# Kernel tuning notes

Hardware: AMD Instinct MI355X
Metric: run time of the kernel (lower is better)

The kernel has to match this reference:

```python
import jax, jax.numpy as jnp
import numpy as np
import math

B, T, D, H = 2, 2048, 1024, 16
HD = D // H
EPS = 1e-5


def layer_norm(x, gamma, beta):
    mu = jnp.mean(x, axis=-1, keepdims=True)
    var = jnp.mean(jnp.square(x - mu), axis=-1, keepdims=True)
    return (x - mu) * jax.lax.rsqrt(var + EPS) * gamma + beta


def setup_inputs() -> dict:
    key = jax.random.key(0)
    ks = jax.random.split(key, 12)
    s = 0.02
    return {
        "x": jax.random.normal(ks[0], (B, T, D), dtype=jnp.float32),
        # weights stored [in, out] (apply as x @ W)
        "w_qkv": jax.random.normal(ks[1], (D, 3 * D), dtype=jnp.float32) * s,
        "w_out": jax.random.normal(ks[2], (D, D), dtype=jnp.float32) * s,
        "w_ff1": jax.random.normal(ks[3], (D, 4 * D), dtype=jnp.float32) * s,
        "b_ff1": jnp.zeros((4 * D,), dtype=jnp.float32),
        "w_ff2": jax.random.normal(ks[4], (4 * D, D), dtype=jnp.float32) * s,
        "b_ff2": jnp.zeros((D,), dtype=jnp.float32),
        "g1": jnp.ones((D,), dtype=jnp.float32),
        "be1": jnp.zeros((D,), dtype=jnp.float32),
        "g2": jnp.ones((D,), dtype=jnp.float32),
        "be2": jnp.zeros((D,), dtype=jnp.float32),
    }


def reference(x, w_qkv, w_out, w_ff1, b_ff1, w_ff2, b_ff2, g1, be1, g2, be2):
    residual = x
    xn = layer_norm(x, g1, be1)
    qkv = (xn @ w_qkv).reshape(B, T, 3, H, HD)
    q, k, v = jnp.moveaxis(qkv, 2, 0)          # each [B, T, H, HD]
    scale = 1.0 / math.sqrt(HD)
    attn = jnp.einsum("bqhd,bkhd->bhqk", q, k) * scale  # [B,H,T,T]
    attn = jax.nn.softmax(attn, axis=-1)
    out = jnp.einsum("bhqk,bkhd->bqhd", attn, v).reshape(B, T, D)
    out = out @ w_out
    x = residual + out
    residual = x
    xn = layer_norm(x, g2, be2)
    h = jax.nn.gelu(xn @ w_ff1 + b_ff1, approximate=False)  # torch nn.GELU = exact erf
    x = residual + (h @ w_ff2 + b_ff2)
    return x
```

## Files before the change

### kernel.cpp

```cpp
#include <hip/hip_runtime.h>
#include <math.h>

#define Bc 2
#define Tc 2048
#define Dc 1024
#define Hc 16
#define HDc 64
#define Mc (Bc * Tc)

typedef __attribute__((ext_vector_type(4))) float f32x4;
typedef __attribute__((ext_vector_type(8))) short bf16x8;

__device__ __forceinline__ unsigned short f2bf(float f) {
  unsigned int u = __float_as_uint(f);
  u += 0x7fff + ((u >> 16) & 1);
  return (unsigned short)(u >> 16);
}

__device__ __forceinline__ void gload16(const void* g, void* l) {
  __builtin_amdgcn_global_load_lds((const __attribute__((address_space(1))) unsigned int*)g,
                                   (__attribute__((address_space(3))) unsigned int*)l, 16, 0, 0);
}

__global__ __launch_bounds__(256) void wconv_kernel(const float* __restrict__ W,
                                                    unsigned short* __restrict__ Wt,
                                                    int K, int N) {
  __shared__ float tile[64][65];
  const int t = threadIdx.x;
  const int kt = blockIdx.y * 64, nt = blockIdx.x * 64;
#pragma unroll
  for (int p = 0; p < 4; p++) {
    int kr = p * 16 + (t >> 4);
    int nc = (t & 15) * 4;
    float4 v = *(const float4*)&W[(size_t)(kt + kr) * N + nt + nc];
    tile[kr][nc] = v.x; tile[kr][nc + 1] = v.y; tile[kr][nc + 2] = v.z; tile[kr][nc + 3] = v.w;
  }
  __syncthreads();
  const int nr = t >> 2, kc = (t & 3) * 16;
  unsigned int u[8];
#pragma unroll
  for (int i = 0; i < 8; i++)
    u[i] = (unsigned int)f2bf(tile[kc + 2 * i][nr]) | ((unsigned int)f2bf(tile[kc + 2 * i + 1][nr]) << 16);
  uint4 w0; w0.x = u[0]; w0.y = u[1]; w0.z = u[2]; w0.w = u[3];
  uint4 w1; w1.x = u[4]; w1.y = u[5]; w1.z = u[6]; w1.w = u[7];
  *(uint4*)&Wt[(size_t)(nt + nr) * K + kt + kc] = w0;
  *(uint4*)&Wt[(size_t)(nt + nr) * K + kt + kc + 8] = w1;
}

__global__ __launch_bounds__(256) void ln_kernel(const float* __restrict__ x,
                                                 const float* __restrict__ g,
                                                 const float* __restrict__ be,
                                                 unsigned short* __restrict__ out) {
  const int row = blockIdx.x;
  const int t = threadIdx.x;
  const float4* xp = (const float4*)(x + (size_t)row * Dc);
  float4 v = xp[t];
  float s = v.x + v.y + v.z + v.w;
  float s2 = v.x * v.x + v.y * v.y + v.z * v.z + v.w * v.w;
#pragma unroll
  for (int off = 32; off; off >>= 1) {
    s += __shfl_down(s, off);
    s2 += __shfl_down(s2, off);
  }
  __shared__ float rs[4], rs2[4];
  if ((t & 63) == 0) { rs[t >> 6] = s; rs2[t >> 6] = s2; }
  __syncthreads();
  float S = rs[0] + rs[1] + rs[2] + rs[3];
  float S2 = rs2[0] + rs2[1] + rs2[2] + rs2[3];
  float mean = S * (1.0f / Dc);
  float var = S2 * (1.0f / Dc) - mean * mean;
  float rstd = rsqrtf(var + 1e-5f);
  float4 gv = ((const float4*)g)[t];
  float4 bv = ((const float4*)be)[t];
  float o0 = (v.x - mean) * rstd * gv.x + bv.x;
  float o1 = (v.y - mean) * rstd * gv.y + bv.y;
  float o2 = (v.z - mean) * rstd * gv.z + bv.z;
  float o3 = (v.w - mean) * rstd * gv.w + bv.w;
  uint2 pk;
  pk.x = (unsigned int)f2bf(o0) | ((unsigned int)f2bf(o1) << 16);
  pk.y = (unsigned int)f2bf(o2) | ((unsigned int)f2bf(o3) << 16);
  *(uint2*)(out + (size_t)row * Dc + t * 4) = pk;
}

#define GBM 128
#define GBN 128
#define GBK 32

__global__ __launch_bounds__(256) void gemm_bf16(const unsigned short* __restrict__ A,
                                                 const unsigned short* __restrict__ Wt,
                                                 const float* __restrict__ bias,
                                                 const float* __restrict__ resid,
                                                 float* __restrict__ C,
                                                 unsigned short* __restrict__ aux,
                                                 int M, int N, int K, int flags) {
  __shared__ alignas(16) unsigned short As[GBM][GBK];
  __shared__ alignas(16) unsigned short Bs[GBN][GBK];
  const int t = threadIdx.x;
  const int lane = t & 63, wave = t >> 6;
  const int wr = wave >> 1, wc = wave & 1;
  const int c = lane & 15, g = lane >> 4;
  const int row0 = blockIdx.y * GBM, col0 = blockIdx.x * GBN;

  f32x4 acc[4][4];
#pragma unroll
  for (int m = 0; m < 4; m++)
#pragma unroll
    for (int n = 0; n < 4; n++) acc[m][n] = (f32x4){0.f, 0.f, 0.f, 0.f};

  char* AsB = (char*)&As[0][0];
  char* BsB = (char*)&Bs[0][0];
  const int l0 = t, l1 = t + 256;
  const int lds0 = wave * 1024, lds1 = wave * 1024 + 4096;

  for (int k0 = 0; k0 < K; k0 += GBK) {
    gload16(A + (size_t)(row0 + (l0 >> 2)) * K + k0 + (l0 & 3) * 8, AsB + lds0);
    gload16(A + (size_t)(row0 + (l1 >> 2)) * K + k0 + (l1 & 3) * 8, AsB + lds1);
    gload16(Wt + (size_t)(col0 + (l0 >> 2)) * K + k0 + (l0 & 3) * 8, BsB + lds0);
    gload16(Wt + (size_t)(col0 + (l1 >> 2)) * K + k0 + (l1 & 3) * 8, BsB + lds1);
    __syncthreads();
    bf16x8 af[4], bfv[4];
#pragma unroll
    for (int m = 0; m < 4; m++) af[m] = *(const bf16x8*)(AsB + (wr * 64 + m * 16 + c) * 64 + g * 16);
#pragma unroll
    for (int n = 0; n < 4; n++) bfv[n] = *(const bf16x8*)(BsB + (wc * 64 + n * 16 + c) * 64 + g * 16);
#pragma unroll
    for (int m = 0; m < 4; m++)
#pragma unroll
      for (int n = 0; n < 4; n++)
        acc[m][n] = __builtin_amdgcn_mfma_f32_16x16x32_bf16(af[m], bfv[n], acc[m][n], 0, 0, 0);
    __syncthreads();
  }

#pragma unroll
  for (int m = 0; m < 4; m++) {
    const int row = row0 + wr * 64 + m * 16 + g * 4;
#pragma unroll
    for (int n = 0; n < 4; n++) {
      const int col = col0 + wc * 64 + n * 16 + c;
      const float bi = (flags & 1) ? bias[col] : 0.0f;
#pragma unroll
      for (int r = 0; r < 4; r++) {
        float v = acc[m][n][r] + bi;
        if (flags & 2) v = 0.5f * v * (1.0f + erff(v * 0.70710678118654752f));
        if (flags & 4) v += resid[(size_t)(row + r) * N + col];
        if (flags & 16) {
          int rr = row + r;
          int b = rr >> 11, tt = rr & 2047;
          int s = col >> 10, wcol = col & 1023;
          int h = wcol >> 6, f = wcol & 63;
          size_t base = ((size_t)(b * Hc + h)) * 131072;
          unsigned short bv = f2bf(v);
          if (s == 0) {
            aux[base + (size_t)tt * HDc + f] = bv;
          } else if (s == 1) {
            aux[4194304 + base + (size_t)(tt >> 4) * 1024 + (f >> 3) * 128 + (tt & 15) * 8 + (f & 7)] = bv;
          } else {
            int kk = tt & 63;
            aux[8388608 + base + (size_t)(tt >> 6) * 4096 + (f >> 4) * 1024 +
                ((kk >> 5) & 1) * 512 + ((kk >> 3) & 3) * 128 + (f & 15) * 8 + (kk & 7)] = bv;
          }
        } else if (flags & 8) {
          aux[(size_t)(row + r) * N + col] = f2bf(v);
        } else {
          C[(size_t)(row + r) * N + col] = v;
        }
      }
    }
  }
}

__global__ __launch_bounds__(256, 4) void fattn(const unsigned short* __restrict__ Qb,
                                                const unsigned short* __restrict__ KF,
                                                const unsigned short* __restrict__ VF,
                                                unsigned short* __restrict__ Ob) {
  __shared__ alignas(16) unsigned short P[4][16][64];
  const int t = threadIdx.x, wave = t >> 6, lane = t & 63;
  const int c = lane & 15, g = lane >> 4;
  const int bid = blockIdx.x;
  const int bh = ((bid & 7) << 2) | ((bid >> 3) & 3);
  const int qt = bid >> 5;
  const int q0 = qt * 64 + wave * 16;

  const unsigned short* Qp = Qb + ((size_t)bh * Tc + q0) * HDc;
  const unsigned short* Kp = KF + (size_t)bh * 131072;
  const unsigned short* Vp = VF + (size_t)bh * 131072;
  char* Pw = (char*)&P[wave][0][0];

  const bf16x8 qf0 = *(const bf16x8*)(Qp + c * HDc + g * 8);
  const bf16x8 qf1 = *(const bf16x8*)(Qp + c * HDc + 32 + g * 8);

  const f32x4 z = {0.f, 0.f, 0.f, 0.f};
  f32x4 o[4] = {z, z, z, z};
  float m[4] = {-3e38f, -3e38f, -3e38f, -3e38f};
  float l[4] = {0.f, 0.f, 0.f, 0.f};
  float minm = -3e38f;
  const float Cs = 0.125f * 1.4426950408889634f;
  const int xc = ((c & 7) << 4) ^ ((c & 8) << 2);
  const int lofs = lane * 8;

  auto loadK = [&](int kt, bf16x8 (&K)[4][2]) {
    const unsigned short* kb = Kp + (kt >> 4) * 1024 + lofs;
#pragma unroll
    for (int i = 0; i < 4; i++) {
      K[i][0] = *(const bf16x8*)(kb + i * 1024);
      K[i][1] = *(const bf16x8*)(kb + i * 1024 + 512);
    }
  };

  auto tile = [&](int kt, bf16x8 (&K)[4][2]) {
    f32x4 s[4];
#pragma unroll
    for (int i = 0; i < 4; i++) {
      s[i] = __builtin_amdgcn_mfma_f32_16x16x32_bf16(qf0, K[i][0], z, 0, 0, 0);
      s[i] = __builtin_amdgcn_mfma_f32_16x16x32_bf16(qf1, K[i][1], s[i], 0, 0, 0);
    }
    const unsigned short* vb = Vp + (kt >> 6) * 4096 + lofs;
    bf16x8 v0[4], v1[4];
#pragma unroll
    for (int d4 = 0; d4 < 4; d4++) {
      v0[d4] = *(const bf16x8*)(vb + d4 * 1024);
      v1[d4] = *(const bf16x8*)(vb + d4 * 1024 + 512);
    }
#pragma unroll
    for (int i = 0; i < 4; i++)
#pragma unroll
      for (int r = 0; r < 4; r++) s[i][r] *= Cs;

    float LM = s[0][0];
#pragma unroll
    for (int i = 0; i < 4; i++)
#pragma unroll
      for (int r = 0; r < 4; r++) LM = fmaxf(LM, s[i][r]);

    if (!__all(LM <= minm + 8.0f)) {
#pragma unroll
      for (int r = 0; r < 4; r++) {
        float rm = fmaxf(fmaxf(s[0][r], s[1][r]), fmaxf(s[2][r], s[3][r]));
        rm = fmaxf(rm, __shfl_xor(rm, 1));
        rm = fmaxf(rm, __shfl_xor(rm, 2));
        rm = fmaxf(rm, __shfl_xor(rm, 4));
        rm = fmaxf(rm, __shfl_xor(rm, 8));
        float nm = fmaxf(m[r], rm);
        float ef = exp2f(m[r] - nm);
        m[r] = nm;
        l[r] *= ef;
        o[0][r] *= ef; o[1][r] *= ef; o[2][r] *= ef; o[3][r] *= ef;
      }
      minm = fminf(fminf(m[0], m[1]), fminf(m[2], m[3]));
    }

#pragma unroll
    for (int r = 0; r < 4; r++) {
      const int rw = g * 4 + r;
      const int xr = ((rw & 7) << 4) ^ ((rw & 8) << 2);
      float p0 = exp2f(s[0][r] - m[r]);
      float p1 = exp2f(s[1][r] - m[r]);
      float p2 = exp2f(s[2][r] - m[r]);
      float p3 = exp2f(s[3][r] - m[r]);
      l[r] += (p0 + p1) + (p2 + p3);
      *(unsigned short*)(Pw + rw * 128 + ((c * 2) ^ xr))      = f2bf(p0);
      *(unsigned short*)(Pw + rw * 128 + ((32 + c * 2) ^ xr)) = f2bf(p1);
      *(unsigned short*)(Pw + rw * 128 + ((64 + c * 2) ^ xr)) = f2bf(p2);
      *(unsigned short*)(Pw + rw * 128 + ((96 + c * 2) ^ xr)) = f2bf(p3);
    }

    const bf16x8 pf0 = *(const bf16x8*)(Pw + c * 128 + ((g * 16) ^ xc));
    const bf16x8 pf1 = *(const bf16x8*)(Pw + c * 128 + ((64 + g * 16) ^ xc));
#pragma unroll
    for (int d4 = 0; d4 < 4; d4++) {
      o[d4] = __builtin_amdgcn_mfma_f32_16x16x32_bf16(pf0, v0[d4], o[d4], 0, 0, 0);
      o[d4] = __builtin_amdgcn_mfma_f32_16x16x32_bf16(pf1, v1[d4], o[d4], 0, 0, 0);
    }
  };

  bf16x8 kA[4][2], kB[4][2];
  loadK(0, kA);
  for (int kt = 0; kt < Tc; kt += 128) {
    loadK(kt + 64, kB);
    tile(kt, kA);
    loadK((kt + 128) & (Tc - 1), kA);
    tile(kt + 64, kB);
  }

  float linv[4];
#pragma unroll
  for (int r = 0; r < 4; r++) {
    float L = l[r];
    L += __shfl_xor(L, 1); L += __shfl_xor(L, 2); L += __shfl_xor(L, 4); L += __shfl_xor(L, 8);
    linv[r] = 1.0f / L;
  }
  const int b = bh >> 4, h = bh & 15;
#pragma unroll
  for (int r = 0; r < 4; r++) {
    size_t rowoff = ((size_t)b * Tc + q0 + g * 4 + r) * Dc + h * HDc + c;
    Ob[rowoff + 0]  = f2bf(o[0][r] * linv[r]);
    Ob[rowoff + 16] = f2bf(o[1][r] * linv[r]);
    Ob[rowoff + 32] = f2bf(o[2][r] * linv[r]);
    Ob[rowoff + 48] = f2bf(o[3][r] * linv[r]);
  }
}

extern "C" void kernel_launch(void* const* d_in, const int* in_sizes, int n_in,
                              void* d_out, int out_size, void* d_ws, size_t ws_size,
                              hipStream_t stream) {
  const float* x     = (const float*)d_in[0];
  const float* w_qkv = (const float*)d_in[1];
  const float* w_out = (const float*)d_in[2];
  const float* w_ff1 = (const float*)d_in[3];
  const float* b_ff1 = (const float*)d_in[4];
  const float* w_ff2 = (const float*)d_in[5];
  const float* b_ff2 = (const float*)d_in[6];
  const float* g1    = (const float*)d_in[7];
  const float* be1   = (const float*)d_in[8];
  const float* g2    = (const float*)d_in[9];
  const float* be2   = (const float*)d_in[10];

  char* ws = (char*)d_ws;
  unsigned short* qkvb  = (unsigned short*)ws;
  unsigned short* xn    = (unsigned short*)(ws + ((size_t)24 << 20));
  unsigned short* Ob    = (unsigned short*)(ws + ((size_t)32 << 20));
  unsigned short* hbuf  = (unsigned short*)(ws + ((size_t)40 << 20));
  unsigned short* wqkvT = (unsigned short*)(ws + ((size_t)72 << 20));
  unsigned short* woutT = (unsigned short*)(ws + ((size_t)78 << 20));
  unsigned short* wff1T = (unsigned short*)(ws + ((size_t)80 << 20));
  unsigned short* wff2T = (unsigned short*)(ws + ((size_t)88 << 20));
  float* x2 = (float*)d_out;

  dim3 blk(256);
  wconv_kernel<<<dim3(48, 16), blk, 0, stream>>>(w_qkv, wqkvT, Dc, 3 * Dc);
  wconv_kernel<<<dim3(16, 16), blk, 0, stream>>>(w_out, woutT, Dc, Dc);
  wconv_kernel<<<dim3(64, 16), blk, 0, stream>>>(w_ff1, wff1T, Dc, 4 * Dc);
  wconv_kernel<<<dim3(16, 64), blk, 0, stream>>>(w_ff2, wff2T, 4 * Dc, Dc);

  ln_kernel<<<Mc, blk, 0, stream>>>(x, g1, be1, xn);
  gemm_bf16<<<dim3(24, 32), blk, 0, stream>>>(xn, wqkvT, nullptr, nullptr, nullptr, qkvb,
                                              Mc, 3 * Dc, Dc, 16);
  fattn<<<dim3(1024), blk, 0, stream>>>(qkvb, qkvb + 4194304, qkvb + 8388608, Ob);
  gemm_bf16<<<dim3(8, 32), blk, 0, stream>>>(Ob, woutT, nullptr, x, x2, nullptr,
                                             Mc, Dc, Dc, 4);
  ln_kernel<<<Mc, blk, 0, stream>>>(x2, g2, be2, xn);
  gemm_bf16<<<dim3(32, 32), blk, 0, stream>>>(xn, wff1T, b_ff1, nullptr, nullptr, hbuf,
                                              Mc, 4 * Dc, Dc, 1 | 2 | 8);
  gemm_bf16<<<dim3(8, 32), blk, 0, stream>>>(hbuf, wff2T, b_ff2, x2, (float*)d_out, nullptr,
                                             Mc, Dc, 4 * Dc, 1 | 4);
}
```

Baseline: 523.9 us.

## Double-buffer GEMM LDS, add XCD-aware block mapping, smaller N=1024 tiles, fuse weight conversion

The GEMM now double-buffers its LDS tiles, issuing the next K-slice's global-to-LDS loads before computing on the current one, and drops one barrier per iteration. Blocks are remapped on a 1D grid so each XCD gets contiguous column groups, aimed at better L2 reuse. The two N=1024 GEMMs use a 64-row tile to launch more blocks and fill the GPU. The four weight-conversion launches are merged into one kernel. Doubling LDS per block may reduce occupancy. With a single barrier, the prefetch into the other buffer could race with waves still reading it from the previous iteration.

Result: faster. 457.4 us (-12.7%).

```diff
diff --git a/kernel.cpp b/kernel.cpp
--- a/kernel.cpp
+++ b/kernel.cpp
@@ -22,12 +22,19 @@
                                    (__attribute__((address_space(3))) unsigned int*)l, 16, 0, 0);
 }
 
-__global__ __launch_bounds__(256) void wconv_kernel(const float* __restrict__ W,
-                                                    unsigned short* __restrict__ Wt,
-                                                    int K, int N) {
+__global__ __launch_bounds__(256) void wconv_all(const float* __restrict__ w0, const float* __restrict__ w1,
+                                                 const float* __restrict__ w2, const float* __restrict__ w3,
+                                                 unsigned short* __restrict__ o0, unsigned short* __restrict__ o1,
+                                                 unsigned short* __restrict__ o2, unsigned short* __restrict__ o3) {
   __shared__ float tile[64][65];
+  int bid = blockIdx.x;
+  const float* W; unsigned short* Wt; int K, N, tx;
+  if (bid < 768)       { W = w0; Wt = o0; K = 1024; N = 3072; tx = 48; }
+  else if (bid < 1024) { bid -= 768;  W = w1; Wt = o1; K = 1024; N = 1024; tx = 16; }
+  else if (bid < 2048) { bid -= 1024; W = w2; Wt = o2; K = 1024; N = 4096; tx = 64; }
+  else                 { bid -= 2048; W = w3; Wt = o3; K = 4096; N = 1024; tx = 16; }
+  const int kt = (bid / tx) * 64, nt = (bid % tx) * 64;
   const int t = threadIdx.x;
-  const int kt = blockIdx.y * 64, nt = blockIdx.x * 64;
 #pragma unroll
   for (int p = 0; p < 4; p++) {
     int kr = p * 16 + (t >> 4);
@@ -41,10 +48,10 @@
 #pragma unroll
   for (int i = 0; i < 8; i++)
     u[i] = (unsigned int)f2bf(tile[kc + 2 * i][nr]) | ((unsigned int)f2bf(tile[kc + 2 * i + 1][nr]) << 16);
-  uint4 w0; w0.x = u[0]; w0.y = u[1]; w0.z = u[2]; w0.w = u[3];
-  uint4 w1; w1.x = u[4]; w1.y = u[5]; w1.z = u[6]; w1.w = u[7];
-  *(uint4*)&Wt[(size_t)(nt + nr) * K + kt + kc] = w0;
-  *(uint4*)&Wt[(size_t)(nt + nr) * K + kt + kc + 8] = w1;
+  uint4 q0; q0.x = u[0]; q0.y = u[1]; q0.z = u[2]; q0.w = u[3];
+  uint4 q1; q1.x = u[4]; q1.y = u[5]; q1.z = u[6]; q1.w = u[7];
+  *(uint4*)&Wt[(size_t)(nt + nr) * K + kt + kc] = q0;
+  *(uint4*)&Wt[(size_t)(nt + nr) * K + kt + kc + 8] = q1;
 }
 
 __global__ __launch_bounds__(256) void ln_kernel(const float* __restrict__ x,
@@ -82,10 +89,7 @@
   *(uint2*)(out + (size_t)row * Dc + t * 4) = pk;
 }
 
-#define GBM 128
-#define GBN 128
-#define GBK 32
-
+template<int BM>
 __global__ __launch_bounds__(256) void gemm_bf16(const unsigned short* __restrict__ A,
                                                  const unsigned short* __restrict__ Wt,
                                                  const float* __restrict__ bias,
@@ -93,50 +97,74 @@
                                                  float* __restrict__ C,
                                                  unsigned short* __restrict__ aux,
                                                  int M, int N, int K, int flags) {
-  __shared__ alignas(16) unsigned short As[GBM][GBK];
-  __shared__ alignas(16) unsigned short Bs[GBN][GBK];
+  constexpr int BN = 128;
+  constexpr int NW = (BM == 128) ? 2 : 4;
+  constexpr int WN = BN / NW;
+  constexpr int NFR = WN / 16;
+  constexpr int ALOADS = BM / 64;
+  __shared__ alignas(16) unsigned short As[2][BM][32];
+  __shared__ alignas(16) unsigned short Bs[2][BN][32];
   const int t = threadIdx.x;
   const int lane = t & 63, wave = t >> 6;
-  const int wr = wave >> 1, wc = wave & 1;
+  const int wr = (BM == 128) ? (wave >> 1) : 0;
+  const int wc = (BM == 128) ? (wave & 1) : wave;
   const int c = lane & 15, g = lane >> 4;
-  const int row0 = blockIdx.y * GBM, col0 = blockIdx.x * GBN;
-
-  f32x4 acc[4][4];
+
+  const int gx = N / BN;
+  const int sw = gx >> 3;
+  const int bid = blockIdx.x;
+  const int xcd = bid & 7, lid = bid >> 3;
+  const int lx = xcd * sw + lid % sw;
+  const int ly = lid / sw;
+  const int row0 = ly * BM, col0 = lx * BN;
+
+  f32x4 acc[4][NFR];
 #pragma unroll
   for (int m = 0; m < 4; m++)
 #pragma unroll
-    for (int n = 0; n < 4; n++) acc[m][n] = (f32x4){0.f, 0.f, 0.f, 0.f};
-
-  char* AsB = (char*)&As[0][0];
-  char* BsB = (char*)&Bs[0][0];
-  const int l0 = t, l1 = t + 256;
-  const int lds0 = wave * 1024, lds1 = wave * 1024 + 4096;
-
-  for (int k0 = 0; k0 < K; k0 += GBK) {
-    gload16(A + (size_t)(row0 + (l0 >> 2)) * K + k0 + (l0 & 3) * 8, AsB + lds0);
-    gload16(A + (size_t)(row0 + (l1 >> 2)) * K + k0 + (l1 & 3) * 8, AsB + lds1);
-    gload16(Wt + (size_t)(col0 + (l0 >> 2)) * K + k0 + (l0 & 3) * 8, BsB + lds0);
-    gload16(Wt + (size_t)(col0 + (l1 >> 2)) * K + k0 + (l1 & 3) * 8, BsB + lds1);
+    for (int n = 0; n < NFR; n++) acc[m][n] = (f32x4){0.f, 0.f, 0.f, 0.f};
+
+  auto stage = [&](int k0, int buf) {
+    char* AsB = (char*)&As[buf][0][0] + wave * 1024;
+    char* BsB = (char*)&Bs[buf][0][0] + wave * 1024;
+#pragma unroll
+    for (int i = 0; i < ALOADS; i++) {
+      int l = t + 256 * i;
+      gload16(A + (size_t)(row0 + (l >> 2)) * K + k0 + (l & 3) * 8, AsB + i * 4096);
+    }
+#pragma unroll
+    for (int i = 0; i < 2; i++) {
+      int l = t + 256 * i;
+      gload16(Wt + (size_t)(col0 + (l >> 2)) * K + k0 + (l & 3) * 8, BsB + i * 4096);
+    }
+  };
+
+  const int nk = K / 32;
+  stage(0, 0);
+  for (int ki = 0; ki < nk; ki++) {
+    const int buf = ki & 1;
     __syncthreads();
-    bf16x8 af[4], bfv[4];
-#pragma unroll
-    for (int m = 0; m < 4; m++) af[m] = *(const bf16x8*)(AsB + (wr * 64 + m * 16 + c) * 64 + g * 16);
-#pragma unroll
-    for (int n = 0; n < 4; n++) bfv[n] = *(const bf16x8*)(BsB + (wc * 64 + n * 16 + c) * 64 + g * 16);
+    if (ki + 1 < nk) stage((ki + 1) * 32, buf ^ 1);
+    const char* Ab = (const char*)&As[buf][0][0];
+    const char* Bb = (const char*)&Bs[buf][0][0];
+    bf16x8 af[4], bfv[NFR];
+#pragma unroll
+    for (int m = 0; m < 4; m++) af[m] = *(const bf16x8*)(Ab + (wr * 64 + m * 16 + c) * 64 + g * 16);
+#pragma unroll
+    for (int n = 0; n < NFR; n++) bfv[n] = *(const bf16x8*)(Bb + (wc * WN + n * 16 + c) * 64 + g * 16);
 #pragma unroll
     for (int m = 0; m < 4; m++)
 #pragma unroll
-      for (int n = 0; n < 4; n++)
+      for (int n = 0; n < NFR; n++)
         acc[m][n] = __builtin_amdgcn_mfma_f32_16x16x32_bf16(af[m], bfv[n], acc[m][n], 0, 0, 0);
-    __syncthreads();
   }
 
 #pragma unroll
   for (int m = 0; m < 4; m++) {
     const int row = row0 + wr * 64 + m * 16 + g * 4;
 #pragma unroll
-    for (int n = 0; n < 4; n++) {
-      const int col = col0 + wc * 64 + n * 16 + c;
+    for (int n = 0; n < NFR; n++) {
+      const int col = col0 + wc * WN + n * 16 + c;
       const float bi = (flags & 1) ? bias[col] : 0.0f;
 #pragma unroll
       for (int r = 0; r < 4; r++) {
@@ -327,20 +355,17 @@
   float* x2 = (float*)d_out;
 
   dim3 blk(256);
-  wconv_kernel<<<dim3(48, 16), blk, 0, stream>>>(w_qkv, wqkvT, Dc, 3 * Dc);
-  wconv_kernel<<<dim3(16, 16), blk, 0, stream>>>(w_out, woutT, Dc, Dc);
-  wconv_kernel<<<dim3(64, 16), blk, 0, stream>>>(w_ff1, wff1T, Dc, 4 * Dc);
-  wconv_kernel<<<dim3(16, 64), blk, 0, stream>>>(w_ff2, wff2T, 4 * Dc, Dc);
+  wconv_all<<<3072, blk, 0, stream>>>(w_qkv, w_out, w_ff1, w_ff2, wqkvT, woutT, wff1T, wff2T);
 
   ln_kernel<<<Mc, blk, 0, stream>>>(x, g1, be1, xn);
-  gemm_bf16<<<dim3(24, 32), blk, 0, stream>>>(xn, wqkvT, nullptr, nullptr, nullptr, qkvb,
-                                              Mc, 3 * Dc, Dc, 16);
+  gemm_bf16<128><<<768, blk, 0, stream>>>(xn, wqkvT, nullptr, nullptr, nullptr, qkvb,
+                                          Mc, 3 * Dc, Dc, 16);
   fattn<<<dim3(1024), blk, 0, stream>>>(qkvb, qkvb + 4194304, qkvb + 8388608, Ob);
-  gemm_bf16<<<dim3(8, 32), blk, 0, stream>>>(Ob, woutT, nullptr, x, x2, nullptr,
-                                             Mc, Dc, Dc, 4);
+  gemm_bf16<64><<<512, blk, 0, stream>>>(Ob, woutT, nullptr, x, x2, nullptr,
+                                         Mc, Dc, Dc, 4);
   ln_kernel<<<Mc, blk, 0, stream>>>(x2, g2, be2, xn);
-  gemm_bf16<<<dim3(32, 32), blk, 0, stream>>>(xn, wff1T, b_ff1, nullptr, nullptr, hbuf,
-                                              Mc, 4 * Dc, Dc, 1 | 2 | 8);
-  gemm_bf16<<<dim3(8, 32), blk, 0, stream>>>(hbuf, wff2T, b_ff2, x2, (float*)d_out, nullptr,
-                                             Mc, Dc, 4 * Dc, 1 | 4);
-}
+  gemm_bf16<128><<<1024, blk, 0, stream>>>(xn, wff1T, b_ff1, nullptr, nullptr, hbuf,
+                                           Mc, 4 * Dc, Dc, 1 | 2 | 8);
+  gemm_bf16<64><<<512, blk, 0, stream>>>(hbuf, wff2T, b_ff2, x2, (float*)d_out, nullptr,
+                                         Mc, Dc, 4 * Dc, 1 | 4);
+}
```
